# Kernel optimization log

Measured on AMD Instinct MI355X. Metric: run time of the kernel, lower is better.

The kernel has to match this reference:

```python
import jax, jax.numpy as jnp
import numpy as np

LUT_SIZE = 65536
OUT_F = 4096
IN_F = 4096
B, S = 4, 2048


def setup_inputs() -> dict:
    key = jax.random.key(0)
    k_x, k_idx, k_lut = jax.random.split(key, 3)
    x = jax.random.normal(k_x, (B, S, IN_F), dtype=jnp.float32)
    grid_indices = jax.random.randint(k_idx, (OUT_F, IN_F), 0, LUT_SIZE, dtype=jnp.int32)
    lut = jax.random.normal(k_lut, (LUT_SIZE,), dtype=jnp.float32)
    scale = jnp.ones((OUT_F, 1), dtype=jnp.float32)
    return {"x": x, "grid_indices": grid_indices, "lut": lut, "scale": scale}


def reference(x, grid_indices, lut, scale):
    # Dequantize: LUT gather per weight element, per-output-row scale.
    weights = lut[grid_indices] * scale  # [out_f, in_f]
    # F.linear(x, weights) == x @ weights.T
    return jnp.einsum('bsi,oi->bso', x, weights)
```

## Files before the change

### kernel.cpp

```cpp
#include <hip/hip_runtime.h>
#include <hip/hip_bf16.h>


typedef __bf16 bf16x8 __attribute__((ext_vector_type(8)));
typedef float f32x4 __attribute__((ext_vector_type(4)));
typedef float f32x16 __attribute__((ext_vector_type(16)));

#define AS1(p) ((__attribute__((address_space(1))) void*)(p))
#define AS3(p) ((__attribute__((address_space(3))) void*)(p))

static constexpr int M_DIM = 8192;
static constexpr int N_DIM = 4096;
static constexpr int K_DIM = 4096;

__global__ __launch_bounds__(1024) void dequant_w_kernel(
    const int* __restrict__ idx, const float* __restrict__ lut,
    int4* __restrict__ wout) {
  __shared__ unsigned short lut_s[32768];
  const int tid = threadIdx.x;
  const int4* i4 = (const int4*)idx;

  int4 ia[4], ib[4];
  union { unsigned short u[8]; int4 q; } o[4];
#pragma unroll
  for (int it = 0; it < 4; ++it) {
    const int w = blockIdx.x * 4096 + it * 1024 + tid;
    ia[it] = i4[2 * w];
    ib[it] = i4[2 * w + 1];
  }

  for (int i = tid; i < 32768; i += 1024) {
    __bf16 b = (__bf16)lut[i];
    lut_s[i] = *(const unsigned short*)&b;
  }
  __syncthreads();
#pragma unroll
  for (int it = 0; it < 4; ++it) {
    if (ia[it].x < 32768) o[it].u[0] = lut_s[ia[it].x];
    if (ia[it].y < 32768) o[it].u[1] = lut_s[ia[it].y];
    if (ia[it].z < 32768) o[it].u[2] = lut_s[ia[it].z];
    if (ia[it].w < 32768) o[it].u[3] = lut_s[ia[it].w];
    if (ib[it].x < 32768) o[it].u[4] = lut_s[ib[it].x];
    if (ib[it].y < 32768) o[it].u[5] = lut_s[ib[it].y];
    if (ib[it].z < 32768) o[it].u[6] = lut_s[ib[it].z];
    if (ib[it].w < 32768) o[it].u[7] = lut_s[ib[it].w];
  }
  __syncthreads();

  for (int i = tid; i < 32768; i += 1024) {
    __bf16 b = (__bf16)lut[32768 + i];
    lut_s[i] = *(const unsigned short*)&b;
  }
  __syncthreads();
#pragma unroll
  for (int it = 0; it < 4; ++it) {
    if (ia[it].x >= 32768) o[it].u[0] = lut_s[ia[it].x - 32768];
    if (ia[it].y >= 32768) o[it].u[1] = lut_s[ia[it].y - 32768];
    if (ia[it].z >= 32768) o[it].u[2] = lut_s[ia[it].z - 32768];
    if (ia[it].w >= 32768) o[it].u[3] = lut_s[ia[it].w - 32768];
    if (ib[it].x >= 32768) o[it].u[4] = lut_s[ib[it].x - 32768];
    if (ib[it].y >= 32768) o[it].u[5] = lut_s[ib[it].y - 32768];
    if (ib[it].z >= 32768) o[it].u[6] = lut_s[ib[it].z - 32768];
    if (ib[it].w >= 32768) o[it].u[7] = lut_s[ib[it].w - 32768];
    const int w = blockIdx.x * 4096 + it * 1024 + tid;
    wout[w] = o[it].q;
  }
}

__global__ __launch_bounds__(256) void cvt_x_kernel(
    const float4* __restrict__ x, int4* __restrict__ aout) {
  const int t = blockIdx.x * 256 + threadIdx.x;
  const float4 a = x[2 * t];
  const float4 b = x[2 * t + 1];
  union { bf16x8 v; int4 q; } u;
  u.v[0] = (__bf16)a.x;  u.v[1] = (__bf16)a.y;
  u.v[2] = (__bf16)a.z;  u.v[3] = (__bf16)a.w;
  u.v[4] = (__bf16)b.x;  u.v[5] = (__bf16)b.y;
  u.v[6] = (__bf16)b.z;  u.v[7] = (__bf16)b.w;
  aout[t] = u.q;
}

__global__ __launch_bounds__(256, 2) void gemm_bt_kernel(
    const unsigned short* __restrict__ A, const unsigned short* __restrict__ Bw,
    const float* __restrict__ scale, float* __restrict__ C) {
  __shared__ __align__(16) unsigned short As[256 * 32];
  __shared__ __align__(16) unsigned short Bs[128 * 32];

  const int tid  = threadIdx.x;
  const int lane = tid & 63;
  const int wave = tid >> 6;
  const int lm = lane & 31;
  const int lh = lane >> 5;
  const int wrow = (wave >> 1) * 128;
  const int wcol = (wave & 1) * 64;
  const size_t n_blk = (size_t)blockIdx.x * 128;
  const size_t m_blk = (size_t)blockIdx.y * 256;

  const size_t rowb = (size_t)K_DIM * 2;
  const char* Ag = (const char*)(A + m_blk * K_DIM);
  const char* Bg = (const char*)(Bw + n_blk * K_DIM);
  const char* AsB = (const char*)As;
  const char* BsB = (const char*)Bs;

  const int sRow  = tid >> 2;
  const int sSlot = tid & 3;

  f32x16 acc[4][2] = {};

  for (int kb = 0; kb < K_DIM; kb += 32) {
    const char* Agk = Ag + (size_t)kb * 2;
    const char* Bgk = Bg + (size_t)kb * 2;
#pragma unroll
    for (int it = 0; it < 4; ++it) {
      const int r = it * 64 + sRow;
      const int c = sSlot ^ ((r >> 1) & 3);
      __builtin_amdgcn_global_load_lds(AS1(Agk + (size_t)r * rowb + c * 16),
                                       AS3((char*)AsB + it * 4096 + tid * 16),
                                       16, 0, 0);
    }
#pragma unroll
    for (int it = 0; it < 2; ++it) {
      const int r = it * 64 + sRow;
      const int c = sSlot ^ ((r >> 1) & 3);
      __builtin_amdgcn_global_load_lds(AS1(Bgk + (size_t)r * rowb + c * 16),
                                       AS3((char*)BsB + it * 4096 + tid * 16),
                                       16, 0, 0);
    }
    __syncthreads();

#pragma unroll
    for (int s = 0; s < 2; ++s) {
      bf16x8 bfr[2];
#pragma unroll
      for (int j = 0; j < 2; ++j) {
        const int r = wcol + j * 32 + lm;
        const int p = (2 * s + lh) ^ ((r >> 1) & 3);
        bfr[j] = *(const bf16x8*)(BsB + r * 64 + p * 16);
      }
#pragma unroll
      for (int i = 0; i < 4; ++i) {
        const int r = wrow + i * 32 + lm;
        const int p = (2 * s + lh) ^ ((r >> 1) & 3);
        const bf16x8 af = *(const bf16x8*)(AsB + r * 64 + p * 16);
#pragma unroll
        for (int j = 0; j < 2; ++j)
          acc[i][j] = __builtin_amdgcn_mfma_f32_32x32x16_bf16(
              af, bfr[j], acc[i][j], 0, 0, 0);
      }
    }
    __syncthreads();
  }

  const float sc0 = scale[n_blk + wcol + lm];
  const float sc1 = scale[n_blk + wcol + 32 + lm];
#pragma unroll
  for (int i = 0; i < 4; ++i) {
    const size_t mb = m_blk + wrow + i * 32 + 4 * lh;
#pragma unroll
    for (int g = 0; g < 4; ++g) {
#pragma unroll
      for (int rr = 0; rr < 4; ++rr) {
        const size_t m = mb + 8 * g + rr;
        float* Crow = C + m * N_DIM + n_blk + wcol + lm;
        Crow[0]  = acc[i][0][g * 4 + rr] * sc0;
        Crow[32] = acc[i][1][g * 4 + rr] * sc1;
      }
    }
  }
}

extern "C" void kernel_launch(void* const* d_in, const int* in_sizes, int n_in,
                              void* d_out, int out_size, void* d_ws, size_t ws_size,
                              hipStream_t stream) {
  const float* x     = (const float*)d_in[0];
  const int*   gidx  = (const int*)d_in[1];
  const float* lut   = (const float*)d_in[2];
  const float* scale = (const float*)d_in[3];
  float* out = (float*)d_out;

  unsigned short* wbf = (unsigned short*)d_ws;
  unsigned short* abf = wbf + (size_t)N_DIM * K_DIM;

  dequant_w_kernel<<<dim3(512), dim3(1024), 0, stream>>>(gidx, lut, (int4*)wbf);
  cvt_x_kernel<<<dim3((M_DIM * (size_t)K_DIM) / 8 / 256), dim3(256), 0, stream>>>(
      (const float4*)x, (int4*)abf);
  gemm_bt_kernel<<<dim3(N_DIM / 128, M_DIM / 256), dim3(256), 0, stream>>>(
      abf, wbf, scale, out);
}
```

Baseline: 595.6 us.

## Replace GEMM with 8-wave 256x256 double-buffered pipelined kernel and vectorize LUT staging

Replaces the single-buffered 256x128 GEMM with a 512-thread kernel on 256x256 output tiles. It uses a K-step of 64, double-buffered LDS (128 KB dynamic), a finer XOR swizzle, a workgroup remap for L2 locality, and quarter-tile interleaving of global_load_lds staging with MFMA issue under manual waitcnt/barrier and setprio control. The goal is to hide global load latency and halve the B-tile reloads per output. The dequant kernel also stages the LUT with float4 loads and 64-bit LDS writes. The tight manual vmcnt accounting and the large LDS footprint limit occupancy to one block per CU and risk subtle synchronisation errors.

```diff
diff --git a/kernel.cpp b/kernel.cpp
--- a/kernel.cpp
+++ b/kernel.cpp
@@ -3,7 +3,6 @@
 
 
 typedef __bf16 bf16x8 __attribute__((ext_vector_type(8)));
-typedef float f32x4 __attribute__((ext_vector_type(4)));
 typedef float f32x16 __attribute__((ext_vector_type(16)));
 
 #define AS1(p) ((__attribute__((address_space(1))) void*)(p))
@@ -19,6 +18,7 @@
   __shared__ unsigned short lut_s[32768];
   const int tid = threadIdx.x;
   const int4* i4 = (const int4*)idx;
+  const float4* lut4 = (const float4*)lut;
 
   int4 ia[4], ib[4];
   union { unsigned short u[8]; int4 q; } o[4];
@@ -29,9 +29,17 @@
     ib[it] = i4[2 * w + 1];
   }
 
-  for (int i = tid; i < 32768; i += 1024) {
-    __bf16 b = (__bf16)lut[i];
-    lut_s[i] = *(const unsigned short*)&b;
+#pragma unroll
+  for (int i8 = 0; i8 < 8; ++i8) {
+    const int c = i8 * 1024 + tid;
+    const float4 f = lut4[c];
+    union { unsigned short u[4]; unsigned long long q; } s;
+    __bf16 b0 = (__bf16)f.x, b1 = (__bf16)f.y, b2 = (__bf16)f.z, b3 = (__bf16)f.w;
+    s.u[0] = *(const unsigned short*)&b0;
+    s.u[1] = *(const unsigned short*)&b1;
+    s.u[2] = *(const unsigned short*)&b2;
+    s.u[3] = *(const unsigned short*)&b3;
+    *(unsigned long long*)&lut_s[4 * c] = s.q;
   }
   __syncthreads();
 #pragma unroll
@@ -47,9 +55,17 @@
   }
   __syncthreads();
 
-  for (int i = tid; i < 32768; i += 1024) {
-    __bf16 b = (__bf16)lut[32768 + i];
-    lut_s[i] = *(const unsigned short*)&b;
+#pragma unroll
+  for (int i8 = 0; i8 < 8; ++i8) {
+    const int c = i8 * 1024 + tid;
+    const float4 f = lut4[8192 + c];
+    union { unsigned short u[4]; unsigned long long q; } s;
+    __bf16 b0 = (__bf16)f.x, b1 = (__bf16)f.y, b2 = (__bf16)f.z, b3 = (__bf16)f.w;
+    s.u[0] = *(const unsigned short*)&b0;
+    s.u[1] = *(const unsigned short*)&b1;
+    s.u[2] = *(const unsigned short*)&b2;
+    s.u[3] = *(const unsigned short*)&b3;
+    *(unsigned long long*)&lut_s[4 * c] = s.q;
   }
   __syncthreads();
 #pragma unroll
@@ -80,88 +96,176 @@
   aout[t] = u.q;
 }
 
-__global__ __launch_bounds__(256, 2) void gemm_bt_kernel(
+
+__device__ __forceinline__ void load_af(bf16x8 af[2][4], const char* p,
+                                        const int ck[4]) {
+#pragma unroll
+  for (int il = 0; il < 2; ++il)
+#pragma unroll
+    for (int t = 0; t < 4; ++t)
+      af[il][t] = *(const bf16x8*)(p + il * 4096 + ck[t]);
+}
+
+__device__ __forceinline__ void load_bf(bf16x8 bf[4], const char* p,
+                                        const int ck[4]) {
+#pragma unroll
+  for (int t = 0; t < 4; ++t)
+    bf[t] = *(const bf16x8*)(p + ck[t]);
+}
+
+template <int HB, int J>
+__device__ __forceinline__ void mma_quad(f32x16 acc[4][2],
+                                         const bf16x8 af[2][4],
+                                         const bf16x8 bf[4]) {
+#pragma unroll
+  for (int t = 0; t < 4; ++t)
+#pragma unroll
+    for (int il = 0; il < 2; ++il)
+      acc[HB * 2 + il][J] = __builtin_amdgcn_mfma_f32_32x32x16_bf16(
+          af[il][t], bf[t], acc[HB * 2 + il][J], 0, 0, 0);
+}
+
+#define BAR __builtin_amdgcn_s_barrier()
+#define VMCNT4 asm volatile("s_waitcnt vmcnt(4)" ::: "memory")
+#define LGKM0                                          \
+  do {                                                 \
+    asm volatile("s_waitcnt lgkmcnt(0)" ::: "memory"); \
+    __builtin_amdgcn_sched_barrier(0);                 \
+  } while (0)
+
+#define ldsA(PI, HB) (lds + (PI) * 32768 + (HB) * 16384 + aBase)
+#define ldsB(PI, JH) (lds + 65536 + (PI) * 32768 + (JH) * 16384 + bBase)
+
+#define STAGE_A(PI, HB, KN)                                                    \
+  do {                                                                         \
+    const size_t gofs = gA0 + (size_t)(HB)*524288 + (size_t)(KN)*2;            \
+    __builtin_amdgcn_global_load_lds(                                          \
+        AS1(Ag + gofs),                                                        \
+        AS3(lds + (PI)*32768 + (HB)*16384 + tid * 16), 16, 0, 0);              \
+    __builtin_amdgcn_global_load_lds(                                          \
+        AS1(Ag + gofs + 1048576),                                              \
+        AS3(lds + (PI)*32768 + (HB)*16384 + 8192 + tid * 16), 16, 0, 0);       \
+  } while (0)
+
+#define STAGE_B(PI, HB, KN)                                                    \
+  do {                                                                         \
+    const size_t gofs = gB0 + (size_t)(HB)*262144 + (size_t)(KN)*2;            \
+    __builtin_amdgcn_global_load_lds(                                          \
+        AS1(Bg + gofs),                                                        \
+        AS3(lds + 65536 + (PI)*32768 + (HB)*16384 + tid * 16), 16, 0, 0);      \
+    __builtin_amdgcn_global_load_lds(                                          \
+        AS1(Bg + gofs + 1048576),                                              \
+        AS3(lds + 65536 + (PI)*32768 + (HB)*16384 + 8192 + tid * 16), 16, 0,   \
+        0);                                                                    \
+  } while (0)
+
+#define TILE(PI, KN)                        \
+  do {                                      \
+                                    \
+    load_af(af, ldsA(PI, 0), ck);           \
+    load_bf(bf, ldsB(PI, 0), ck);           \
+    STAGE_A((PI) ^ 1, 0, KN);               \
+    BAR;                                    \
+    LGKM0;                                  \
+    __builtin_amdgcn_s_setprio(1);          \
+    mma_quad<0, 0>(acc, af, bf);            \
+    __builtin_amdgcn_s_setprio(0);          \
+    VMCNT4;                                 \
+    BAR;                                    \
+                                    \
+    load_bf(bf, ldsB(PI, 1), ck);           \
+    STAGE_B((PI) ^ 1, 0, KN);               \
+    BAR;                                    \
+    LGKM0;                                  \
+    __builtin_amdgcn_s_setprio(1);          \
+    mma_quad<0, 1>(acc, af, bf);            \
+    __builtin_amdgcn_s_setprio(0);          \
+    VMCNT4;                                 \
+    BAR;                                    \
+                                    \
+    load_af(af, ldsA(PI, 1), ck);           \
+    STAGE_B((PI) ^ 1, 1, KN);               \
+    BAR;                                    \
+    LGKM0;                                  \
+    __builtin_amdgcn_s_setprio(1);          \
+    mma_quad<1, 1>(acc, af, bf);            \
+    __builtin_amdgcn_s_setprio(0);          \
+    BAR;                                    \
+                                    \
+    load_bf(bf, ldsB(PI, 0), ck);           \
+    STAGE_A((PI) ^ 1, 1, KN);               \
+    BAR;                                    \
+    LGKM0;                                  \
+    __builtin_amdgcn_s_setprio(1);          \
+    mma_quad<1, 0>(acc, af, bf);            \
+    __builtin_amdgcn_s_setprio(0);          \
+    VMCNT4;                                 \
+    BAR;                                    \
+  } while (0)
+
+__global__ __launch_bounds__(512) void gemm8_kernel(
     const unsigned short* __restrict__ A, const unsigned short* __restrict__ Bw,
     const float* __restrict__ scale, float* __restrict__ C) {
-  __shared__ __align__(16) unsigned short As[256 * 32];
-  __shared__ __align__(16) unsigned short Bs[128 * 32];
-
-  const int tid  = threadIdx.x;
+  extern __shared__ __align__(16) char lds[];
+
+  const int tid = threadIdx.x;
   const int lane = tid & 63;
-  const int wave = tid >> 6;
   const int lm = lane & 31;
   const int lh = lane >> 5;
-  const int wrow = (wave >> 1) * 128;
-  const int wcol = (wave & 1) * 64;
-  const size_t n_blk = (size_t)blockIdx.x * 128;
-  const size_t m_blk = (size_t)blockIdx.y * 256;
-
-  const size_t rowb = (size_t)K_DIM * 2;
+  const int wave = tid >> 6;
+  const int wr = wave >> 2;
+  const int wc = wave & 3;
+
+  int wg = blockIdx.x;
+  wg = ((wg & 7) << 6) | (wg >> 3);
+  const int bx = wg & 15;
+  const int by = wg >> 4;
+  const size_t m_blk = (size_t)by * 256;
+  const size_t n_blk = (size_t)bx * 256;
+
   const char* Ag = (const char*)(A + m_blk * K_DIM);
   const char* Bg = (const char*)(Bw + n_blk * K_DIM);
-  const char* AsB = (const char*)As;
-  const char* BsB = (const char*)Bs;
-
-  const int sRow  = tid >> 2;
-  const int sSlot = tid & 3;
+
+  const int u = tid >> 3;
+  const int cs = (tid & 7) ^ (u & 7);
+  const size_t gA0 = (size_t)u * 8192 + (size_t)cs * 16;
+  const size_t gB0 = (size_t)((u & 31) + ((u >> 5) << 6)) * 8192 +
+                     (size_t)cs * 16;
+
+  const int aBase = (lm + 64 * wr) * 128;
+  const int bBase = (lm + 32 * wc) * 128;
+  int ck[4];
+#pragma unroll
+  for (int t = 0; t < 4; ++t) ck[t] = (((2 * t + lh) ^ (lm & 7)) << 4);
 
   f32x16 acc[4][2] = {};
-
-  for (int kb = 0; kb < K_DIM; kb += 32) {
-    const char* Agk = Ag + (size_t)kb * 2;
-    const char* Bgk = Bg + (size_t)kb * 2;
-#pragma unroll
-    for (int it = 0; it < 4; ++it) {
-      const int r = it * 64 + sRow;
-      const int c = sSlot ^ ((r >> 1) & 3);
-      __builtin_amdgcn_global_load_lds(AS1(Agk + (size_t)r * rowb + c * 16),
-                                       AS3((char*)AsB + it * 4096 + tid * 16),
-                                       16, 0, 0);
-    }
-#pragma unroll
-    for (int it = 0; it < 2; ++it) {
-      const int r = it * 64 + sRow;
-      const int c = sSlot ^ ((r >> 1) & 3);
-      __builtin_amdgcn_global_load_lds(AS1(Bgk + (size_t)r * rowb + c * 16),
-                                       AS3((char*)BsB + it * 4096 + tid * 16),
-                                       16, 0, 0);
-    }
-    __syncthreads();
-
-#pragma unroll
-    for (int s = 0; s < 2; ++s) {
-      bf16x8 bfr[2];
-#pragma unroll
-      for (int j = 0; j < 2; ++j) {
-        const int r = wcol + j * 32 + lm;
-        const int p = (2 * s + lh) ^ ((r >> 1) & 3);
-        bfr[j] = *(const bf16x8*)(BsB + r * 64 + p * 16);
-      }
-#pragma unroll
-      for (int i = 0; i < 4; ++i) {
-        const int r = wrow + i * 32 + lm;
-        const int p = (2 * s + lh) ^ ((r >> 1) & 3);
-        const bf16x8 af = *(const bf16x8*)(AsB + r * 64 + p * 16);
-#pragma unroll
-        for (int j = 0; j < 2; ++j)
-          acc[i][j] = __builtin_amdgcn_mfma_f32_32x32x16_bf16(
-              af, bfr[j], acc[i][j], 0, 0, 0);
-      }
-    }
-    __syncthreads();
-  }
-
-  const float sc0 = scale[n_blk + wcol + lm];
-  const float sc1 = scale[n_blk + wcol + 32 + lm];
+  bf16x8 af[2][4];
+  bf16x8 bf[4];
+
+  STAGE_A(0, 0, 0);
+  STAGE_B(0, 0, 0);
+  STAGE_B(0, 1, 0);
+  STAGE_A(0, 1, 0);
+  VMCNT4;
+  BAR;
+
+  for (int it = 0; it < 32; ++it) {
+    const int kb = it << 7;
+    TILE(0, kb + 64);
+    TILE(1, (kb + 128) & 4095);
+  }
+
+  const float sc0 = scale[n_blk + wc * 64 + lm];
+  const float sc1 = scale[n_blk + wc * 64 + 32 + lm];
 #pragma unroll
   for (int i = 0; i < 4; ++i) {
-    const size_t mb = m_blk + wrow + i * 32 + 4 * lh;
+    const size_t mb = m_blk + wr * 128 + i * 32 + 4 * lh;
 #pragma unroll
     for (int g = 0; g < 4; ++g) {
 #pragma unroll
       for (int rr = 0; rr < 4; ++rr) {
         const size_t m = mb + 8 * g + rr;
-        float* Crow = C + m * N_DIM + n_blk + wcol + lm;
+        float* Crow = C + m * N_DIM + n_blk + wc * 64 + lm;
         Crow[0]  = acc[i][0][g * 4 + rr] * sc0;
         Crow[32] = acc[i][1][g * 4 + rr] * sc1;
       }
@@ -184,6 +288,5 @@
   dequant_w_kernel<<<dim3(512), dim3(1024), 0, stream>>>(gidx, lut, (int4*)wbf);
   cvt_x_kernel<<<dim3((M_DIM * (size_t)K_DIM) / 8 / 256), dim3(256), 0, stream>>>(
       (const float4*)x, (int4*)abf);
-  gemm_bt_kernel<<<dim3(N_DIM / 128, M_DIM / 256), dim3(256), 0, stream>>>(
-      abf, wbf, scale, out);
-}
+  gemm8_kernel<<<dim3(512), dim3(512), 131072, stream>>>(abf, wbf, scale, out);
+}
```

New measurement: 523.2 us. 12.2% less time.
